# Kernel optimization log

Hardware: AMD Instinct MI355X
Metric: run time of the kernel (lower is better)

The kernel has to match this reference:

```python
import jax, jax.numpy as jnp
import numpy as np

WS = (7, 7)          # window size
SS = (3, 3)          # shift size
NUM_HEADS = 6
DIM = 192


def _relative_position_index(ws):
    ch = np.arange(ws[0]); cw = np.arange(ws[1])
    coords = np.stack(np.meshgrid(ch, cw, indexing='ij')).reshape(2, -1)  # [2, N]
    rel = coords[:, :, None] - coords[:, None, :]                          # [2, N, N]
    rel = rel.transpose(1, 2, 0)
    rel[:, :, 0] += ws[0] - 1
    rel[:, :, 1] += ws[1] - 1
    rel[:, :, 0] *= 2 * ws[1] - 1
    return rel.sum(-1).reshape(-1)                                         # [N*N]


def _shift_mask(pH, pW, ws, ss):
    m = np.zeros((pH, pW))
    cnt = 0
    for h0, h1 in ((0, pH - ws[0]), (pH - ws[0], pH - ss[0]), (pH - ss[0], pH)):
        for w0, w1 in ((0, pW - ws[1]), (pW - ws[1], pW - ss[1]), (pW - ss[1], pW)):
            m[h0:h1, w0:w1] = cnt
            cnt += 1
    nw = (pH // ws[0]) * (pW // ws[1])
    N = ws[0] * ws[1]
    m = m.reshape(pH // ws[0], ws[0], pW // ws[1], ws[1]).transpose(0, 2, 1, 3).reshape(nw, N)
    diff = m[:, None, :] - m[:, :, None]
    return np.where(diff != 0, -100.0, 0.0).astype(np.float32)             # [nw, N, N]


def setup_inputs() -> dict:
    key = jax.random.key(0)
    ks = jax.random.split(key, 6)
    B, H, W, C = 16, 112, 112, DIM
    return {
        'x': jax.random.normal(ks[0], (B, H, W, C), dtype=jnp.float32),
        'qkv_weight': jax.random.normal(ks[1], (3 * C, C), dtype=jnp.float32) * 0.02,
        'qkv_bias': jax.random.normal(ks[2], (3 * C,), dtype=jnp.float32) * 0.02,
        'proj_weight': jax.random.normal(ks[3], (C, C), dtype=jnp.float32) * 0.02,
        'proj_bias': jax.random.normal(ks[4], (C,), dtype=jnp.float32) * 0.02,
        'rel_bias_table': jax.random.normal(ks[5], ((2 * WS[0] - 1) * (2 * WS[1] - 1), NUM_HEADS), dtype=jnp.float32) * 0.02,
    }


def reference(x, qkv_weight, qkv_bias, proj_weight, proj_bias, rel_bias_table):
    B, H, W, C = x.shape
    ws, ss, nh = WS, SS, NUM_HEADS
    hd = C // nh
    N = ws[0] * ws[1]

    # pad to multiple of window (static; here pads are 0 but kept for fidelity)
    pad_b = (ws[0] - H % ws[0]) % ws[0]
    pad_r = (ws[1] - W % ws[1]) % ws[1]
    x = jnp.pad(x, ((0, 0), (0, pad_b), (0, pad_r), (0, 0)))
    pH, pW = H + pad_b, W + pad_r
    shifted = sum(ss) > 0 and ws[0] < pH and ws[1] < pW
    if shifted:
        x = jnp.roll(x, shift=(-ss[0], -ss[1]), axis=(1, 2))

    nHw, nWw = pH // ws[0], pW // ws[1]
    nw = nHw * nWw
    # window partition -> [B*nw, N, C]
    xw = x.reshape(B, nHw, ws[0], nWw, ws[1], C).transpose(0, 1, 3, 2, 4, 5)
    xw = xw.reshape(B * nw, N, C)

    # qkv projection
    qkv = xw @ qkv_weight.T + qkv_bias                                     # [Bn, N, 3C]
    qkv = qkv.reshape(B * nw, N, 3, nh, hd).transpose(2, 0, 3, 1, 4)       # [3, Bn, h, N, hd]
    q, k, v = qkv[0], qkv[1], qkv[2]
    q = q * (hd ** -0.5)

    attn = jnp.einsum('bhqd,bhkd->bhqk', q, k)                             # [Bn, h, N, N]

    # relative position bias (static gather indices)
    idx = _relative_position_index(ws)
    bias = rel_bias_table[idx].reshape(N, N, nh).transpose(2, 0, 1)        # [h, N, N]
    attn = attn + bias[None]

    if shifted:
        mask = jnp.asarray(_shift_mask(pH, pW, ws, ss))                    # [nw, N, N]
        attn = attn.reshape(B, nw, nh, N, N) + mask[None, :, None]
        attn = attn.reshape(B * nw, nh, N, N)

    attn = jax.nn.softmax(attn, axis=-1)
    out = jnp.einsum('bhqk,bhkd->bhqd', attn, v)                           # [Bn, h, N, hd]
    out = out.transpose(0, 2, 1, 3).reshape(B * nw, N, C)
    out = out @ proj_weight.T + proj_bias

    # window reverse
    out = out.reshape(B, nHw, nWw, ws[0], ws[1], C).transpose(0, 1, 3, 2, 4, 5)
    out = out.reshape(B, pH, pW, C)
    if shifted:
        out = jnp.roll(out, shift=(ss[0], ss[1]), axis=(1, 2))
    return out[:, :H, :W, :]
```

## Files before the change

### kernel.cpp

```cpp
#include <hip/hip_runtime.h>
#include <cstddef>
#include <cstdint>

typedef __attribute__((ext_vector_type(4))) float f32x4;
typedef __attribute__((ext_vector_type(8))) short s16x8;

constexpr int CC = 192, NHEAD = 6, HD = 32, NTOK = 49, IMG = 112, TOTWIN = 4096;
constexpr int MTOK = TOTWIN * NTOK;
constexpr float QSCALE = 0.17677669529663687f;
constexpr size_t PLANE_U16 = (size_t)TOTWIN * NHEAD * 4 * 64 * 8;
constexpr int WQ_SLOTS = 6 * 36 * 64;
constexpr int WP_SLOTS = 6 * 12 * 64;
constexpr int TBL_N    = 6 * 4 * 64 * 64;

__device__ __forceinline__ unsigned short bfh(float f) {
    unsigned u = __float_as_uint(f);
    return (unsigned short)((u + 0x7FFFu + ((u >> 16) & 1u)) >> 16);
}
__device__ __forceinline__ float bff(unsigned short h) {
    return __uint_as_float(((unsigned)h) << 16);
}
#define MFMA_BF16(acc, a, b) \
    (acc) = __builtin_amdgcn_mfma_f32_16x16x32_bf16((a), (b), (acc), 0, 0, 0)

__device__ __forceinline__ int arow_off_qkv(int m) {
    int win = m / NTOK, tok = m - win * NTOK;
    int b = win >> 8, wib = win & 255;
    int ih = tok / 7, iw = tok - ih * 7;
    int sh = (wib >> 4) * 7 + ih + 3; if (sh >= IMG) sh -= IMG;
    int sw = (wib & 15) * 7 + iw + 3; if (sw >= IMG) sw -= IMG;
    return ((b * IMG + sh) * IMG + sw) * CC;
}

__global__ void prep(const float* __restrict__ wq, const float* __restrict__ wp,
                     const float* __restrict__ rbt,
                     short* __restrict__ wqh, short* __restrict__ wql,
                     short* __restrict__ wph, short* __restrict__ wpl,
                     float* __restrict__ tbl) {
    int i = blockIdx.x * 256 + threadIdx.x;
    if (i < WQ_SLOTS + WP_SLOTS) {
        const float* src; short *dh, *dl; int slot, nfr;
        if (i < WQ_SLOTS) { src = wq; dh = wqh; dl = wql; slot = i; nfr = 36; }
        else              { src = wp; dh = wph; dl = wpl; slot = i - WQ_SLOTS; nfr = 12; }
        int kt = slot / (nfr * 64), rem = slot % (nfr * 64), f = rem >> 6, lane = rem & 63;
        int n = f * 16 + (lane & 15), k = kt * 32 + (lane >> 4) * 8;
        s16x8 hv, lv;
        #pragma unroll
        for (int j = 0; j < 8; ++j) {
            float v = src[n * CC + k + j];
            unsigned short h = bfh(v);
            hv[j] = (short)h; lv[j] = (short)bfh(v - bff(h));
        }
        *reinterpret_cast<s16x8*>(dh + (size_t)slot * 8) = hv;
        *reinterpret_cast<s16x8*>(dl + (size_t)slot * 8) = lv;
    }
    int ti = i - (WQ_SLOTS + WP_SLOTS);
    if (ti >= 0 && ti < TBL_N) {
        int h = ti / (4 * 4096), rem = ti % (4 * 4096), cls = rem >> 12, e = rem & 4095;
        int kr = e >> 6, q = e & 63;
        float v;
        if (kr >= NTOK) v = -1e30f;
        else if (q >= NTOK) v = 0.f;
        else {
            int qh = q / 7, qw = q % 7, kh = kr / 7, kw = kr % 7;
            float b = rbt[((qh - kh + 6) * 13 + (qw - kw + 6)) * NHEAD + h];
            int rq = ((cls >> 1) ? (qh < 4 ? 3 : 6) : 0) + ((cls & 1) ? (qw < 4 ? 1 : 2) : 0);
            int rk = ((cls >> 1) ? (kh < 4 ? 3 : 6) : 0) + ((cls & 1) ? (kw < 4 ? 1 : 2) : 0);
            v = (rq != rk) ? b - 100.f : b;
        }
        tbl[ti] = v;
    }
}

template<int MODE>
__global__ __launch_bounds__(256, 2)
void gemm_swapped(const float* __restrict__ Asrc,
                  const short* __restrict__ Wh, const short* __restrict__ Wl,
                  const float* __restrict__ bias,
                  short* __restrict__ qpl, short* __restrict__ kpl, short* __restrict__ vpl,
                  float* __restrict__ outp) {
    __shared__ s16x8 AhS[512], AlS[512], BhS[768], BlS[768];
    int mt, nblk;
    if (MODE == 0) {
        int bid = blockIdx.x;
        int virt = (bid & 7) * 588 + (bid >> 3);
        mt = virt / 3; nblk = virt - mt * 3;
    } else { mt = blockIdx.x; nblk = 0; }
    const int t = threadIdx.x, w = t >> 6, lane = t & 63, l15 = lane & 15, lc = lane >> 4;
    const int nfr = (MODE == 0) ? 36 : 12;

    const int sl15 = t & 15, slc = (t >> 4) & 3;
    const int m0g = mt * 128 + w * 16 + sl15;
    const int m1g = m0g + 64;
    const size_t abase0 = (size_t)(MODE == 0 ? arow_off_qkv(m0g) : m0g * CC) + slc * 8;
    const size_t abase1 = (size_t)(MODE == 0 ? arow_off_qkv(m1g) : m1g * CC) + slc * 8;

    f32x4 acc[4][6];
    #pragma unroll
    for (int mi = 0; mi < 4; ++mi)
        #pragma unroll
        for (int ni = 0; ni < 6; ++ni) acc[mi][ni] = (f32x4){0.f, 0.f, 0.f, 0.f};

    const int mh = w >> 1, nh = w & 1;

    for (int kt = 0; kt < 6; ++kt) {
        {
            const size_t gb = ((size_t)(kt * nfr) + nblk * 12) * 512;
            #pragma unroll
            for (int u = 0; u < 3; ++u) {
                const int s = t + u * 256;
                BhS[s] = *reinterpret_cast<const s16x8*>(Wh + gb + (size_t)s * 8);
                BlS[s] = *reinterpret_cast<const s16x8*>(Wl + gb + (size_t)s * 8);
            }
        }
        float4 x0 = *reinterpret_cast<const float4*>(Asrc + abase0 + kt * 32);
        float4 x1 = *reinterpret_cast<const float4*>(Asrc + abase0 + kt * 32 + 4);
        float4 y0 = *reinterpret_cast<const float4*>(Asrc + abase1 + kt * 32);
        float4 y1 = *reinterpret_cast<const float4*>(Asrc + abase1 + kt * 32 + 4);
        float xv[8] = {x0.x, x0.y, x0.z, x0.w, x1.x, x1.y, x1.z, x1.w};
        float yv[8] = {y0.x, y0.y, y0.z, y0.w, y1.x, y1.y, y1.z, y1.w};
        s16x8 xh, xl, yh, yl;
        #pragma unroll
        for (int j = 0; j < 8; ++j) {
            unsigned short h0 = bfh(xv[j]); xh[j] = (short)h0; xl[j] = (short)bfh(xv[j] - bff(h0));
            unsigned short h1 = bfh(yv[j]); yh[j] = (short)h1; yl[j] = (short)bfh(yv[j] - bff(h1));
        }
        AhS[t] = xh; AlS[t] = xl; AhS[t + 256] = yh; AlS[t + 256] = yl;
        __syncthreads();

        s16x8 fah[4], fal[4], fbh[6], fbl[6];
        #pragma unroll
        for (int mi = 0; mi < 4; ++mi) {
            fah[mi] = AhS[(mh * 4 + mi) * 64 + lane];
            fal[mi] = AlS[(mh * 4 + mi) * 64 + lane];
        }
        #pragma unroll
        for (int ni = 0; ni < 6; ++ni) {
            fbh[ni] = BhS[(nh * 6 + ni) * 64 + lane];
            fbl[ni] = BlS[(nh * 6 + ni) * 64 + lane];
        }
        #pragma unroll
        for (int mi = 0; mi < 4; ++mi)
            #pragma unroll
            for (int ni = 0; ni < 6; ++ni) MFMA_BF16(acc[mi][ni], fbh[ni], fah[mi]);
        #pragma unroll
        for (int mi = 0; mi < 4; ++mi)
            #pragma unroll
            for (int ni = 0; ni < 6; ++ni) MFMA_BF16(acc[mi][ni], fbh[ni], fal[mi]);
        #pragma unroll
        for (int mi = 0; mi < 4; ++mi)
            #pragma unroll
            for (int ni = 0; ni < 6; ++ni) MFMA_BF16(acc[mi][ni], fbl[ni], fah[mi]);
        __syncthreads();
    }

    #pragma unroll
    for (int mi = 0; mi < 4; ++mi) {
        const int m = mt * 128 + mh * 64 + mi * 16 + l15;
        const int win = m / NTOK, tok = m - win * NTOK;
        if (MODE == 0) {
            const int s = tok >> 5, lcv = (tok >> 3) & 3, jv = tok & 7;
            const int qt = tok >> 4, l15f = tok & 15;
            #pragma unroll
            for (int ni = 0; ni < 6; ++ni) {
                const int cb = nh * 96 + ni * 16 + lc * 4;
                const int head = cb >> 5, d0 = cb & 31;
                const size_t task = (size_t)(win * NHEAD + head);
                float4 b4 = *reinterpret_cast<const float4*>(bias + nblk * 192 + cb);
                float vv[4] = {acc[mi][ni][0] + b4.x, acc[mi][ni][1] + b4.y,
                               acc[mi][ni][2] + b4.z, acc[mi][ni][3] + b4.w};
                if (nblk == 0) {
                    #pragma unroll
                    for (int r = 0; r < 4; ++r) vv[r] *= QSCALE;
                }
                if (nblk < 2) {
                    short* pl = (nblk == 0) ? qpl : kpl;
                    short* dst = pl + (task * 4 + qt) * 512 + (d0 >> 3) * 128 + l15f * 8 + (d0 & 7);
                    uint2 pk;
                    pk.x = (unsigned)bfh(vv[0]) | ((unsigned)bfh(vv[1]) << 16);
                    pk.y = (unsigned)bfh(vv[2]) | ((unsigned)bfh(vv[3]) << 16);
                    *reinterpret_cast<uint2*>(dst) = pk;
                } else {
                    const int niv = d0 >> 4, l15v0 = d0 & 15;
                    size_t vb = ((task * 2 + s) * 2 + niv) * 512 + lcv * 128 + jv;
                    #pragma unroll
                    for (int r = 0; r < 4; ++r)
                        vpl[vb + (size_t)(l15v0 + r) * 8] = (short)bfh(vv[r]);
                }
            }
        } else {
            const int b = win >> 8, wib = win & 255;
            const int ih = tok / 7, iw = tok - ih * 7;
            int fh = (wib >> 4) * 7 + ih + 3; if (fh >= IMG) fh -= IMG;
            int fw = (wib & 15) * 7 + iw + 3; if (fw >= IMG) fw -= IMG;
            float* orow = outp + ((size_t)((b * IMG + fh) * IMG + fw)) * CC;
            #pragma unroll
            for (int ni = 0; ni < 6; ++ni) {
                const int cb = nh * 96 + ni * 16 + lc * 4;
                float4 b4 = *reinterpret_cast<const float4*>(bias + cb);
                float4 vv = {acc[mi][ni][0] + b4.x, acc[mi][ni][1] + b4.y,
                             acc[mi][ni][2] + b4.z, acc[mi][ni][3] + b4.w};
                *reinterpret_cast<float4*>(orow + cb) = vv;
            }
        }
    }
}

__global__ __launch_bounds__(64)
void attn(const short* __restrict__ qpl, const short* __restrict__ kpl,
          const short* __restrict__ vpl, const float* __restrict__ tbl,
          float* __restrict__ Ows) {
    __shared__ unsigned int FR[2048];
    const int win = blockIdx.x, h = blockIdx.y;
    const int lane = threadIdx.x, l15 = lane & 15, lc = lane >> 4;
    const size_t tq = (size_t)(win * NHEAD + h) * 2048;

    s16x8 qf[4], kf[4], vf[2][2];
    #pragma unroll
    for (int qt = 0; qt < 4; ++qt) {
        qf[qt] = *reinterpret_cast<const s16x8*>(qpl + tq + (qt * 64 + lane) * 8);
        kf[qt] = *reinterpret_cast<const s16x8*>(kpl + tq + (qt * 64 + lane) * 8);
    }
    #pragma unroll
    for (int s = 0; s < 2; ++s)
        #pragma unroll
        for (int ni = 0; ni < 2; ++ni)
            vf[s][ni] = *reinterpret_cast<const s16x8*>(vpl + tq + ((s * 2 + ni) * 64 + lane) * 8);

    f32x4 st[4][4];
    #pragma unroll
    for (int kt = 0; kt < 4; ++kt)
        #pragma unroll
        for (int qt = 0; qt < 4; ++qt) {
            st[kt][qt] = (f32x4){0.f, 0.f, 0.f, 0.f};
            MFMA_BF16(st[kt][qt], kf[kt], qf[qt]);
        }

    const int wib = win & 255;
    const int cls = (((wib >> 4) == 15) ? 2 : 0) + (((wib & 15) == 15) ? 1 : 0);
    const float* tb = tbl + ((h * 4 + cls) << 12);
    #pragma unroll
    for (int kt = 0; kt < 4; ++kt)
        #pragma unroll
        for (int qt = 0; qt < 4; ++qt)
            #pragma unroll
            for (int r = 0; r < 4; ++r)
                st[kt][qt][r] += tb[(kt * 16 + lc * 4 + r) * 64 + qt * 16 + l15];

    float inv[4];
    #pragma unroll
    for (int qt = 0; qt < 4; ++qt) {
        float mx = st[0][qt][0];
        #pragma unroll
        for (int kt = 0; kt < 4; ++kt)
            #pragma unroll
            for (int r = 0; r < 4; ++r) mx = fmaxf(mx, st[kt][qt][r]);
        mx = fmaxf(mx, __shfl_xor(mx, 16));
        mx = fmaxf(mx, __shfl_xor(mx, 32));
        float sum = 0.f;
        #pragma unroll
        for (int kt = 0; kt < 4; ++kt)
            #pragma unroll
            for (int r = 0; r < 4; ++r) {
                float e = __expf(st[kt][qt][r] - mx);
                st[kt][qt][r] = e; sum += e;
            }
        sum += __shfl_xor(sum, 16);
        sum += __shfl_xor(sum, 32);
        inv[qt] = 1.0f / sum;
    }

    #pragma unroll
    for (int kt = 0; kt < 4; ++kt)
        #pragma unroll
        for (int qt = 0; qt < 4; ++qt) {
            float p0 = st[kt][qt][0] * inv[qt], p1 = st[kt][qt][1] * inv[qt];
            float p2 = st[kt][qt][2] * inv[qt], p3 = st[kt][qt][3] * inv[qt];
            unsigned pk01 = (unsigned)bfh(p0) | ((unsigned)bfh(p1) << 16);
            unsigned pk23 = (unsigned)bfh(p2) | ((unsigned)bfh(p3) << 16);
            int tl = ((kt & 1) * 2 + (lc >> 1)) * 16 + l15;
            int base = (((kt >> 1) * 4 + qt) * 64 + tl) * 4 + (lc & 1) * 2;
            FR[base] = pk01; FR[base + 1] = pk23;
        }
    __syncthreads();
    s16x8 pa[2][4];
    #pragma unroll
    for (int s = 0; s < 2; ++s)
        #pragma unroll
        for (int qt = 0; qt < 4; ++qt)
            pa[s][qt] = *reinterpret_cast<const s16x8*>(&FR[((s * 4 + qt) * 64 + lane) * 4]);

    f32x4 o[4][2];
    #pragma unroll
    for (int qt = 0; qt < 4; ++qt)
        #pragma unroll
        for (int ni = 0; ni < 2; ++ni) o[qt][ni] = (f32x4){0.f, 0.f, 0.f, 0.f};
    #pragma unroll
    for (int s = 0; s < 2; ++s)
        #pragma unroll
        for (int qt = 0; qt < 4; ++qt)
            #pragma unroll
            for (int ni = 0; ni < 2; ++ni)
                MFMA_BF16(o[qt][ni], pa[s][qt], vf[s][ni]);

    const size_t obase = (size_t)win * NTOK * CC + h * HD;
    #pragma unroll
    for (int qt = 0; qt < 4; ++qt)
        #pragma unroll
        for (int r = 0; r < 4; ++r) {
            int qrow = qt * 16 + lc * 4 + r;
            if (qrow < NTOK) {
                #pragma unroll
                for (int ni = 0; ni < 2; ++ni)
                    Ows[obase + (size_t)qrow * CC + ni * 16 + l15] = o[qt][ni][r];
            }
        }
}

extern "C" void kernel_launch(void* const* d_in, const int* in_sizes, int n_in,
                              void* d_out, int out_size, void* d_ws, size_t ws_size,
                              hipStream_t stream) {
    const float* x     = (const float*)d_in[0];
    const float* qkvw  = (const float*)d_in[1];
    const float* qkvb  = (const float*)d_in[2];
    const float* projw = (const float*)d_in[3];
    const float* projb = (const float*)d_in[4];
    const float* relb  = (const float*)d_in[5];

    char* ws = (char*)d_ws;
    short* qpl = (short*)ws;
    short* kpl = qpl + PLANE_U16;
    short* vpl = kpl + PLANE_U16;
    float* Ows = (float*)(vpl + PLANE_U16);
    short* wqh = (short*)(Ows + (size_t)MTOK * CC);
    short* wql = wqh + (size_t)WQ_SLOTS * 8;
    short* wph = wql + (size_t)WQ_SLOTS * 8;
    short* wpl_ = wph + (size_t)WP_SLOTS * 8;
    float* tbl = (float*)(wpl_ + (size_t)WP_SLOTS * 8);

    prep<<<456, 256, 0, stream>>>(qkvw, projw, relb, wqh, wql, wph, wpl_, tbl);
    gemm_swapped<0><<<4704, 256, 0, stream>>>(x, wqh, wql, qkvb, qpl, kpl, vpl, nullptr);
    attn<<<dim3(TOTWIN, NHEAD), 64, 0, stream>>>(qpl, kpl, vpl, tbl, Ows);
    gemm_swapped<1><<<1568, 256, 0, stream>>>(Ows, wph, wpl_, projb, nullptr, nullptr, nullptr,
                                              (float*)d_out);
}
```

Baseline: 598.5 us.

## Pre-split inputs to bf16 hi/lo planes and stage GEMM tiles via direct global-to-LDS loads

Adds an xsplit pass that converts x into bf16 high/low planes once. The attention kernel now writes its output as bf16 hi/lo planes as well, so both GEMMs take pre-split operands instead of converting fp32 per tile. The GEMMs load A and W tiles with global_load_lds straight into shared memory, skipping register staging. Separately, the bias/mask table is relaid out in MFMA fragment order so attention can read it with vector loads, and the V fragment loads are moved to after the softmax. The cost is an extra full pass over x and hi/lo workspace buffers the size of x for both x and the attention output.

```diff
diff --git a/kernel.cpp b/kernel.cpp
--- a/kernel.cpp
+++ b/kernel.cpp
@@ -4,14 +4,16 @@
 
 typedef __attribute__((ext_vector_type(4))) float f32x4;
 typedef __attribute__((ext_vector_type(8))) short s16x8;
+typedef __attribute__((ext_vector_type(4))) unsigned short u16x4;
 
 constexpr int CC = 192, NHEAD = 6, HD = 32, NTOK = 49, IMG = 112, TOTWIN = 4096;
 constexpr int MTOK = TOTWIN * NTOK;
+constexpr int NX   = MTOK * CC;
 constexpr float QSCALE = 0.17677669529663687f;
 constexpr size_t PLANE_U16 = (size_t)TOTWIN * NHEAD * 4 * 64 * 8;
 constexpr int WQ_SLOTS = 6 * 36 * 64;
 constexpr int WP_SLOTS = 6 * 12 * 64;
-constexpr int TBL_N    = 6 * 4 * 64 * 64;
+constexpr int TBL_N    = 6 * 4 * 4096;
 
 __device__ __forceinline__ unsigned short bfh(float f) {
     unsigned u = __float_as_uint(f);
@@ -22,6 +24,11 @@
 }
 #define MFMA_BF16(acc, a, b) \
     (acc) = __builtin_amdgcn_mfma_f32_16x16x32_bf16((a), (b), (acc), 0, 0, 0)
+
+__device__ __forceinline__ void gll16(const void* g, void* l) {
+    __builtin_amdgcn_global_load_lds((const __attribute__((address_space(1))) unsigned int*)g,
+                                     (__attribute__((address_space(3))) unsigned int*)l, 16, 0, 0);
+}
 
 __device__ __forceinline__ int arow_off_qkv(int m) {
     int win = m / NTOK, tok = m - win * NTOK;
@@ -30,6 +37,23 @@
     int sh = (wib >> 4) * 7 + ih + 3; if (sh >= IMG) sh -= IMG;
     int sw = (wib & 15) * 7 + iw + 3; if (sw >= IMG) sw -= IMG;
     return ((b * IMG + sh) * IMG + sw) * CC;
+}
+
+__global__ void xsplit(const float* __restrict__ x, unsigned short* __restrict__ xh,
+                       unsigned short* __restrict__ xl) {
+    const int N4 = NX / 4;
+    for (int i = blockIdx.x * blockDim.x + threadIdx.x; i < N4; i += gridDim.x * blockDim.x) {
+        float4 v = reinterpret_cast<const float4*>(x)[i];
+        float f[4] = {v.x, v.y, v.z, v.w};
+        u16x4 hv, lv;
+        #pragma unroll
+        for (int c = 0; c < 4; ++c) {
+            unsigned short h = bfh(f[c]);
+            hv[c] = h; lv[c] = bfh(f[c] - bff(h));
+        }
+        *reinterpret_cast<u16x4*>(xh + (size_t)i * 4) = hv;
+        *reinterpret_cast<u16x4*>(xl + (size_t)i * 4) = lv;
+    }
 }
 
 __global__ void prep(const float* __restrict__ wq, const float* __restrict__ wp,
@@ -56,13 +80,14 @@
     }
     int ti = i - (WQ_SLOTS + WP_SLOTS);
     if (ti >= 0 && ti < TBL_N) {
-        int h = ti / (4 * 4096), rem = ti % (4 * 4096), cls = rem >> 12, e = rem & 4095;
-        int kr = e >> 6, q = e & 63;
+        int h = ti / 16384, rem = ti % 16384, cls = rem >> 12, e = rem & 4095;
+        int r = e & 3, lane = (e >> 2) & 63, qt = (e >> 8) & 3, kt = e >> 10;
+        int k = kt * 16 + (lane >> 4) * 4 + r, q = qt * 16 + (lane & 15);
         float v;
-        if (kr >= NTOK) v = -1e30f;
+        if (k >= NTOK) v = -1e30f;
         else if (q >= NTOK) v = 0.f;
         else {
-            int qh = q / 7, qw = q % 7, kh = kr / 7, kw = kr % 7;
+            int qh = q / 7, qw = q % 7, kh = k / 7, kw = k % 7;
             float b = rbt[((qh - kh + 6) * 13 + (qw - kw + 6)) * NHEAD + h];
             int rq = ((cls >> 1) ? (qh < 4 ? 3 : 6) : 0) + ((cls & 1) ? (qw < 4 ? 1 : 2) : 0);
             int rk = ((cls >> 1) ? (kh < 4 ? 3 : 6) : 0) + ((cls & 1) ? (kw < 4 ? 1 : 2) : 0);
@@ -74,7 +99,7 @@
 
 template<int MODE>
 __global__ __launch_bounds__(256, 2)
-void gemm_swapped(const float* __restrict__ Asrc,
+void gemm_swapped(const unsigned short* __restrict__ Ah, const unsigned short* __restrict__ Al,
                   const short* __restrict__ Wh, const short* __restrict__ Wl,
                   const float* __restrict__ bias,
                   short* __restrict__ qpl, short* __restrict__ kpl, short* __restrict__ vpl,
@@ -89,11 +114,10 @@
     const int t = threadIdx.x, w = t >> 6, lane = t & 63, l15 = lane & 15, lc = lane >> 4;
     const int nfr = (MODE == 0) ? 36 : 12;
 
-    const int sl15 = t & 15, slc = (t >> 4) & 3;
-    const int m0g = mt * 128 + w * 16 + sl15;
-    const int m1g = m0g + 64;
-    const size_t abase0 = (size_t)(MODE == 0 ? arow_off_qkv(m0g) : m0g * CC) + slc * 8;
-    const size_t abase1 = (size_t)(MODE == 0 ? arow_off_qkv(m1g) : m1g * CC) + slc * 8;
+    const int mA0 = mt * 128 + w * 16 + l15;
+    const int mA1 = mA0 + 64;
+    const size_t a0 = (size_t)(MODE == 0 ? arow_off_qkv(mA0) : mA0 * CC) + lc * 8;
+    const size_t a1 = (size_t)(MODE == 0 ? arow_off_qkv(mA1) : mA1 * CC) + lc * 8;
 
     f32x4 acc[4][6];
     #pragma unroll
@@ -104,28 +128,16 @@
     const int mh = w >> 1, nh = w & 1;
 
     for (int kt = 0; kt < 6; ++kt) {
-        {
-            const size_t gb = ((size_t)(kt * nfr) + nblk * 12) * 512;
-            #pragma unroll
-            for (int u = 0; u < 3; ++u) {
-                const int s = t + u * 256;
-                BhS[s] = *reinterpret_cast<const s16x8*>(Wh + gb + (size_t)s * 8);
-                BlS[s] = *reinterpret_cast<const s16x8*>(Wl + gb + (size_t)s * 8);
-            }
-        }
-        float4 x0 = *reinterpret_cast<const float4*>(Asrc + abase0 + kt * 32);
-        float4 x1 = *reinterpret_cast<const float4*>(Asrc + abase0 + kt * 32 + 4);
-        float4 y0 = *reinterpret_cast<const float4*>(Asrc + abase1 + kt * 32);
-        float4 y1 = *reinterpret_cast<const float4*>(Asrc + abase1 + kt * 32 + 4);
-        float xv[8] = {x0.x, x0.y, x0.z, x0.w, x1.x, x1.y, x1.z, x1.w};
-        float yv[8] = {y0.x, y0.y, y0.z, y0.w, y1.x, y1.y, y1.z, y1.w};
-        s16x8 xh, xl, yh, yl;
-        #pragma unroll
-        for (int j = 0; j < 8; ++j) {
-            unsigned short h0 = bfh(xv[j]); xh[j] = (short)h0; xl[j] = (short)bfh(xv[j] - bff(h0));
-            unsigned short h1 = bfh(yv[j]); yh[j] = (short)h1; yl[j] = (short)bfh(yv[j] - bff(h1));
-        }
-        AhS[t] = xh; AlS[t] = xl; AhS[t + 256] = yh; AlS[t + 256] = yl;
+        gll16(Ah + a0 + kt * 32, &AhS[w * 64]);
+        gll16(Al + a0 + kt * 32, &AlS[w * 64]);
+        gll16(Ah + a1 + kt * 32, &AhS[(w + 4) * 64]);
+        gll16(Al + a1 + kt * 32, &AlS[(w + 4) * 64]);
+        #pragma unroll
+        for (int u = 0; u < 3; ++u) {
+            const size_t gs = ((size_t)((kt * nfr + nblk * 12 + w * 3 + u) * 64) + lane) * 8;
+            gll16(Wh + gs, &BhS[(w * 3 + u) * 64]);
+            gll16(Wl + gs, &BlS[(w * 3 + u) * 64]);
+        }
         __syncthreads();
 
         s16x8 fah[4], fal[4], fbh[6], fbl[6];
@@ -209,23 +221,18 @@
 __global__ __launch_bounds__(64)
 void attn(const short* __restrict__ qpl, const short* __restrict__ kpl,
           const short* __restrict__ vpl, const float* __restrict__ tbl,
-          float* __restrict__ Ows) {
+          unsigned short* __restrict__ oh, unsigned short* __restrict__ ol) {
     __shared__ unsigned int FR[2048];
     const int win = blockIdx.x, h = blockIdx.y;
     const int lane = threadIdx.x, l15 = lane & 15, lc = lane >> 4;
     const size_t tq = (size_t)(win * NHEAD + h) * 2048;
 
-    s16x8 qf[4], kf[4], vf[2][2];
+    s16x8 qf[4], kf[4];
     #pragma unroll
     for (int qt = 0; qt < 4; ++qt) {
         qf[qt] = *reinterpret_cast<const s16x8*>(qpl + tq + (qt * 64 + lane) * 8);
         kf[qt] = *reinterpret_cast<const s16x8*>(kpl + tq + (qt * 64 + lane) * 8);
     }
-    #pragma unroll
-    for (int s = 0; s < 2; ++s)
-        #pragma unroll
-        for (int ni = 0; ni < 2; ++ni)
-            vf[s][ni] = *reinterpret_cast<const s16x8*>(vpl + tq + ((s * 2 + ni) * 64 + lane) * 8);
 
     f32x4 st[4][4];
     #pragma unroll
@@ -242,10 +249,10 @@
     #pragma unroll
     for (int kt = 0; kt < 4; ++kt)
         #pragma unroll
-        for (int qt = 0; qt < 4; ++qt)
-            #pragma unroll
-            for (int r = 0; r < 4; ++r)
-                st[kt][qt][r] += tb[(kt * 16 + lc * 4 + r) * 64 + qt * 16 + l15];
+        for (int qt = 0; qt < 4; ++qt) {
+            f32x4 tv = *reinterpret_cast<const f32x4*>(tb + kt * 1024 + qt * 256 + lane * 4);
+            st[kt][qt] += tv;
+        }
 
     float inv[4];
     #pragma unroll
@@ -269,6 +276,13 @@
         sum += __shfl_xor(sum, 32);
         inv[qt] = 1.0f / sum;
     }
+
+    s16x8 vf[2][2];
+    #pragma unroll
+    for (int s = 0; s < 2; ++s)
+        #pragma unroll
+        for (int ni = 0; ni < 2; ++ni)
+            vf[s][ni] = *reinterpret_cast<const s16x8*>(vpl + tq + ((s * 2 + ni) * 64 + lane) * 8);
 
     #pragma unroll
     for (int kt = 0; kt < 4; ++kt)
@@ -311,8 +325,13 @@
             int qrow = qt * 16 + lc * 4 + r;
             if (qrow < NTOK) {
                 #pragma unroll
-                for (int ni = 0; ni < 2; ++ni)
-                    Ows[obase + (size_t)qrow * CC + ni * 16 + l15] = o[qt][ni][r];
+                for (int ni = 0; ni < 2; ++ni) {
+                    size_t off = obase + (size_t)qrow * CC + ni * 16 + l15;
+                    float val = o[qt][ni][r];
+                    unsigned short hh = bfh(val);
+                    oh[off] = hh;
+                    ol[off] = bfh(val - bff(hh));
+                }
             }
         }
 }
@@ -331,16 +350,20 @@
     short* qpl = (short*)ws;
     short* kpl = qpl + PLANE_U16;
     short* vpl = kpl + PLANE_U16;
-    float* Ows = (float*)(vpl + PLANE_U16);
-    short* wqh = (short*)(Ows + (size_t)MTOK * CC);
-    short* wql = wqh + (size_t)WQ_SLOTS * 8;
-    short* wph = wql + (size_t)WQ_SLOTS * 8;
+    unsigned short* oh = (unsigned short*)(vpl + PLANE_U16);
+    unsigned short* ol = oh + (size_t)NX;
+    unsigned short* xh = ol + (size_t)NX;
+    unsigned short* xl = xh + (size_t)NX;
+    short* wqh  = (short*)(xl + (size_t)NX);
+    short* wql  = wqh + (size_t)WQ_SLOTS * 8;
+    short* wph  = wql + (size_t)WQ_SLOTS * 8;
     short* wpl_ = wph + (size_t)WP_SLOTS * 8;
-    float* tbl = (float*)(wpl_ + (size_t)WP_SLOTS * 8);
-
+    float* tbl  = (float*)(wpl_ + (size_t)WP_SLOTS * 8);
+
+    xsplit<<<2048, 256, 0, stream>>>(x, xh, xl);
     prep<<<456, 256, 0, stream>>>(qkvw, projw, relb, wqh, wql, wph, wpl_, tbl);
-    gemm_swapped<0><<<4704, 256, 0, stream>>>(x, wqh, wql, qkvb, qpl, kpl, vpl, nullptr);
-    attn<<<dim3(TOTWIN, NHEAD), 64, 0, stream>>>(qpl, kpl, vpl, tbl, Ows);
-    gemm_swapped<1><<<1568, 256, 0, stream>>>(Ows, wph, wpl_, projb, nullptr, nullptr, nullptr,
-                                              (float*)d_out);
-}
+    gemm_swapped<0><<<4704, 256, 0, stream>>>(xh, xl, wqh, wql, qkvb, qpl, kpl, vpl, nullptr);
+    attn<<<dim3(TOTWIN, NHEAD), 64, 0, stream>>>(qpl, kpl, vpl, tbl, oh, ol);
+    gemm_swapped<1><<<1568, 256, 0, stream>>>(oh, ol, wph, wpl_, projb,
+                                              nullptr, nullptr, nullptr, (float*)d_out);
+}
```

Result: slower. 658.5 us (+10.0%).
